# Kernel tuning notes

Measured on AMD Instinct MI355X. Metric: run time of the kernel, lower is better.

## Reference

```python
import jax, jax.numpy as jnp
import numpy as np

D = 1024
H = 16
B = 4
L = 1024
EPS = 1e-5


def _ln(x, g, b):
    m = jnp.mean(x, axis=-1, keepdims=True)
    v = jnp.mean((x - m) ** 2, axis=-1, keepdims=True)
    return (x - m) / jnp.sqrt(v + EPS) * g + b


def _bn_eval(x, g, b, mean, var):
    # x: [B, L, C]; per-channel batchnorm in eval mode
    return (x - mean) / jnp.sqrt(var + EPS) * g + b


def setup_inputs() -> dict:
    key = jax.random.key(0)
    ks = jax.random.split(key, 16)
    s = 0.02
    return {
        "q": jax.random.normal(ks[0], (B, L, D), jnp.float32),
        "wq": jax.random.normal(ks[1], (D, D), jnp.float32) * s,
        "bq": jax.random.normal(ks[2], (D,), jnp.float32) * s,
        "wk": jax.random.normal(ks[3], (D, D), jnp.float32) * s,
        "bk": jax.random.normal(ks[4], (D,), jnp.float32) * s,
        "wv": jax.random.normal(ks[5], (D, D), jnp.float32) * s,
        "bv": jax.random.normal(ks[6], (D,), jnp.float32) * s,
        "wo": jax.random.normal(ks[7], (D, D), jnp.float32) * s,
        "bo": jax.random.normal(ks[8], (D,), jnp.float32) * s,
        "w1": jax.random.normal(ks[9], (4 * D, D), jnp.float32) * s,
        "bn1_g": jax.random.uniform(ks[10], (4 * D,), jnp.float32, 0.5, 1.5),
        "bn1_b": jax.random.normal(ks[11], (4 * D,), jnp.float32) * s,
        "bn1_m": jax.random.normal(ks[12], (4 * D,), jnp.float32) * s,
        "bn1_v": jax.random.uniform(ks[13], (4 * D,), jnp.float32, 0.5, 1.5),
        "w2": jax.random.normal(ks[14], (D, 4 * D), jnp.float32) * s,
        "bn2_g": jax.random.uniform(ks[15], (D,), jnp.float32, 0.5, 1.5),
        "bn2_b": jnp.zeros((D,), jnp.float32),
        "bn2_m": jnp.zeros((D,), jnp.float32),
        "bn2_v": jnp.ones((D,), jnp.float32),
        "ln1_g": jnp.ones((D,), jnp.float32),
        "ln1_b": jnp.zeros((D,), jnp.float32),
        "ln3_g": jnp.ones((D,), jnp.float32),
        "ln3_b": jnp.zeros((D,), jnp.float32),
    }


def reference(q, wq, bq, wk, bk, wv, bv, wo, bo,
              w1, bn1_g, bn1_b, bn1_m, bn1_v,
              w2, bn2_g, bn2_b, bn2_m, bn2_v,
              ln1_g, ln1_b, ln3_g, ln3_b):
    hd = D // H
    scale = hd ** -0.5
    # conv1x1 projections == per-token linear: [B,L,D] @ [D,D]^T + bias
    qp = (q @ wq.T + bq).reshape(B, L, H, hd)
    kp = (q @ wk.T + bk).reshape(B, L, H, hd)
    vp = (q @ wv.T + bv).reshape(B, L, H, hd)
    attn = jnp.einsum('blhd,bmhd->bhlm', qp, kp) * scale  # [B,H,L,L]
    attn = jax.nn.softmax(attn, axis=-1)
    out = jnp.einsum('bhlm,bmhd->blhd', attn, vp).reshape(B, L, D)
    out = out @ wo.T + bo
    # post-norm residual block (norm_first=False, use_residual=True)
    x = _ln(q + out, ln1_g, ln1_b)
    # conv-MLP: 1x1 conv -> BN(eval) -> GELU(exact) -> 1x1 conv -> BN(eval)
    h = x @ w1.T                                   # [B,L,4D]
    h = jax.nn.gelu(_bn_eval(h, bn1_g, bn1_b, bn1_m, bn1_v), approximate=False)
    h = _bn_eval(h @ w2.T, bn2_g, bn2_b, bn2_m, bn2_v)  # [B,L,D]
    x = _ln(x + h, ln3_g, ln3_b)
    return x
```

## Files before the change

kernel.cpp:

```cpp
#include <hip/hip_runtime.h>
#include <math.h>

#define EPS 1e-5f

typedef unsigned short ushort_t;
typedef __attribute__((ext_vector_type(8))) __bf16 bf16x8;
typedef __attribute__((ext_vector_type(4))) __bf16 bf16x4;
typedef __attribute__((ext_vector_type(4))) float f32x4;

#define MFMA16(a, b, c) __builtin_amdgcn_mfma_f32_16x16x32_bf16(a, b, c, 0, 0, 0)

#define QSCALE2 0.18033688011112042f

__device__ __forceinline__ unsigned short f2bf(float f) {
  unsigned u = __float_as_uint(f);
  u += 0x7fffu + ((u >> 16) & 1u);
  return (unsigned short)(u >> 16);
}

__device__ __forceinline__ void gload16(const void* g, void* l) {
  __builtin_amdgcn_global_load_lds(
      (__attribute__((address_space(1))) void*)(g),
      (__attribute__((address_space(3))) void*)(l), 16, 0, 0);
}

__global__ __launch_bounds__(256) void cast_all_k(
    const float* __restrict__ wq, const float* __restrict__ wk,
    const float* __restrict__ wv, const float* __restrict__ wo,
    const float* __restrict__ w1, const float* __restrict__ w2,
    const float* __restrict__ q, ushort_t* __restrict__ wqkv,
    ushort_t* __restrict__ wob, ushort_t* __restrict__ w1b,
    ushort_t* __restrict__ w2b, ushort_t* __restrict__ qbf) {
  const int b = blockIdx.x;
  const float* src;
  ushort_t* dst;
  int idx;
  if (b < 2048) {
    const int s = b >> 9;
    src = (s == 0) ? wq : (s == 1) ? wk : (s == 2) ? wv : wo;
    dst = (s == 3) ? wob : wqkv + s * 1048576;
    idx = (b & 511) * 2048 + threadIdx.x * 8;
  } else if (b < 4096) {
    src = w1; dst = w1b; idx = (b - 2048) * 2048 + threadIdx.x * 8;
  } else if (b < 6144) {
    src = w2; dst = w2b; idx = (b - 4096) * 2048 + threadIdx.x * 8;
  } else {
    src = q; dst = qbf; idx = (b - 6144) * 2048 + threadIdx.x * 8;
  }
  float4 a = *(const float4*)(src + idx);
  float4 c = *(const float4*)(src + idx + 4);
  uint4 u;
  u.x = (unsigned)f2bf(a.x) | ((unsigned)f2bf(a.y) << 16);
  u.y = (unsigned)f2bf(a.z) | ((unsigned)f2bf(a.w) << 16);
  u.z = (unsigned)f2bf(c.x) | ((unsigned)f2bf(c.y) << 16);
  u.w = (unsigned)f2bf(c.z) | ((unsigned)f2bf(c.w) << 16);
  *(uint4*)(dst + idx) = u;
}

__global__ __launch_bounds__(256) void bnparam_k(
    const float* __restrict__ g1, const float* __restrict__ b1,
    const float* __restrict__ m1, const float* __restrict__ v1,
    const float* __restrict__ g2, const float* __restrict__ b2,
    const float* __restrict__ m2, const float* __restrict__ v2,
    float* __restrict__ sc1, float* __restrict__ sh1,
    float* __restrict__ sc2, float* __restrict__ sh2) {
  int i = blockIdx.x * 256 + threadIdx.x;
  if (i < 4096) {
    float s = g1[i] * rsqrtf(v1[i] + EPS);
    sc1[i] = s;
    sh1[i] = b1[i] - m1[i] * s;
  } else if (i < 5120) {
    int j = i - 4096;
    float s = g2[j] * rsqrtf(v2[j] + EPS);
    sc2[j] = s;
    sh2[j] = b2[j] - m2[j] * s;
  }
}

template <int KDIM, int EPI, int TM, int TN, int WM, int WN, int NTHR, int GX, int GY>
__global__ __launch_bounds__(NTHR, 2) void gemm_bt(const ushort_t* __restrict__ A,
                                                   const ushort_t* __restrict__ W,
                                                   const float* __restrict__ p0,
                                                   const float* __restrict__ p1,
                                                   const float* __restrict__ p2,
                                                   float* __restrict__ outF,
                                                   ushort_t* __restrict__ outB) {
  constexpr int BM = 16 * TM * WM, BN = 16 * TN * WN;
  constexpr int LDS_STAGE = 2 * (BM + BN) * 128;
  constexpr int LDS_TR = (EPI == 0) ? 128 * 136 * 2 : 0;
  __shared__ alignas(16) char pool[(LDS_STAGE > LDS_TR) ? LDS_STAGE : LDS_TR];
  constexpr int LA = BM * 8 / NTHR;
  constexpr int LB = BN * 8 / NTHR;

  constexpr int NWG = GX * GY;
  const int id = blockIdx.x;
  const int pos = (id & 7) * (NWG / 8) + (id >> 3);
  const int grp = pos / (8 * GX);
  const int rem = pos % (8 * GX);
  const int by = grp * 8 + (rem & 7);
  const int bx = rem >> 3;
  const int bm = by * BM, bn = bx * BN;

  const int tid = threadIdx.x;
  const int lane = tid & 63;
  const int wid = tid >> 6;
  const int wr = wid / WN, wc = wid % WN;
  const int fr = lane & 15;
  const int kg = lane >> 4;

  const char* Ag0 = (const char*)(A + (size_t)bm * KDIM);
  const char* Bg0 = (const char*)(W + (size_t)bn * KDIM);

#define STAGE(bufi, t_)                                                        \
  do {                                                                         \
    const char* Ag = Ag0 + (size_t)(t_)*128;                                   \
    const char* Bg = Bg0 + (size_t)(t_)*128;                                   \
    char* Ab = pool + (bufi) * (BM * 128);                                     \
    char* Bb = pool + 2 * BM * 128 + (bufi) * (BN * 128);                      \
    _Pragma("unroll") for (int li = 0; li < LA; ++li) {                        \
      const int f = li * NTHR + tid;                                           \
      const int row = f >> 3;                                                  \
      const int gl = (f & 7) ^ (row & 7);                                      \
      gload16(Ag + (size_t)row * (KDIM * 2) + gl * 16,                         \
              Ab + (li * NTHR + wid * 64) * 16);                               \
    }                                                                          \
    _Pragma("unroll") for (int li = 0; li < LB; ++li) {                        \
      const int f = li * NTHR + tid;                                           \
      const int row = f >> 3;                                                  \
      const int gl = (f & 7) ^ (row & 7);                                      \
      gload16(Bg + (size_t)row * (KDIM * 2) + gl * 16,                         \
              Bb + (li * NTHR + wid * 64) * 16);                               \
    }                                                                          \
  } while (0)

  f32x4 acc[TM][TN];
#pragma unroll
  for (int i = 0; i < TM; ++i)
#pragma unroll
    for (int j = 0; j < TN; ++j)
#pragma unroll
      for (int r = 0; r < 4; ++r) acc[i][j][r] = 0.f;

  STAGE(0, 0);
  asm volatile("s_waitcnt vmcnt(0)" ::: "memory");
  __builtin_amdgcn_s_barrier();

  constexpr int NT = KDIM / 64;
  for (int t = 0; t < NT; ++t) {
    const int b = t & 1;
    if (t + 1 < NT) STAGE(b ^ 1, t + 1);
    const char* Ac = pool + b * (BM * 128);
    const char* Bc = pool + 2 * BM * 128 + b * (BN * 128);
#pragma unroll
    for (int s = 0; s < 2; ++s) {
      bf16x8 bfv[TN];
#pragma unroll
      for (int nf = 0; nf < TN; ++nf) {
        const int row = wc * (16 * TN) + nf * 16 + fr;
        bfv[nf] = *(const bf16x8*)(Bc + row * 128 + (((s * 4 + kg) ^ (row & 7)) * 16));
      }
#pragma unroll
      for (int mf = 0; mf < TM; ++mf) {
        const int row = wr * (16 * TM) + mf * 16 + fr;
        bf16x8 af = *(const bf16x8*)(Ac + row * 128 + (((s * 4 + kg) ^ (row & 7)) * 16));
#pragma unroll
        for (int nf = 0; nf < TN; ++nf) acc[mf][nf] = MFMA16(af, bfv[nf], acc[mf][nf]);
      }
    }
    asm volatile("s_waitcnt vmcnt(0)" ::: "memory");
    __builtin_amdgcn_s_barrier();
  }
#undef STAGE

  if constexpr (EPI == 0) {
    if (bn < 2048) {
#pragma unroll
      for (int mf = 0; mf < TM; ++mf) {
#pragma unroll
        for (int nf = 0; nf < TN; ++nf) {
#pragma unroll
          for (int r = 0; r < 4; ++r) {
            const int m = bm + wr * (16 * TM) + mf * 16 + kg * 4 + r;
            const int n = bn + wc * (16 * TN) + nf * 16 + fr;
            const int sel = n >> 10;
            const int nl = n & 1023;
            float v = acc[mf][nf][r] + ((sel == 0) ? p0[nl] : p1[nl]);
            if (sel == 0) v *= QSCALE2;
            const int b_ = m >> 10, tok = m & 1023;
            const int h_ = nl >> 6, d_ = nl & 63;
            outB[(size_t)sel * 4194304 + (((size_t)(b_ * 16 + h_) * 1024 + tok) * 64 + d_)] =
                f2bf(v);
          }
        }
      }
    } else {
      __syncthreads();
      ushort_t* T = (ushort_t*)pool;
#pragma unroll
      for (int mf = 0; mf < TM; ++mf) {
#pragma unroll
        for (int nf = 0; nf < TN; ++nf) {
          const int ml = wr * (16 * TM) + mf * 16 + kg * 4;
          const int nl = wc * (16 * TN) + nf * 16 + fr;
          const float bias = p2[(bn & 1023) + nl];
          bf16x4 pw;
#pragma unroll
          for (int r = 0; r < 4; ++r) pw[r] = (__bf16)(acc[mf][nf][r] + bias);
          *(bf16x4*)(T + nl * 136 + ml) = pw;
        }
      }
      __syncthreads();
      const int b_ = bm >> 10;
      const int tokb = bm & 1023;
#pragma unroll
      for (int it = 0; it < 8; ++it) {
        const int g = it * 256 + tid;
        const int nl = g >> 4;
        const int m0 = (g & 15) * 8;
        bf16x8 v = *(const bf16x8*)(T + nl * 136 + m0);
        const int nloc = (bn - 2048) + nl;
        const int h_ = nloc >> 6, d_ = nloc & 63;
        *(bf16x8*)(outB + 8388608 + (((size_t)(b_ * 16 + h_) * 64 + d_) << 10) + tokb + m0) = v;
      }
    }
  } else {
#pragma unroll
    for (int mf = 0; mf < TM; ++mf) {
#pragma unroll
      for (int nf = 0; nf < TN; ++nf) {
#pragma unroll
        for (int r = 0; r < 4; ++r) {
          const int m = bm + wr * (16 * TM) + mf * 16 + kg * 4 + r;
          const int n = bn + wc * (16 * TN) + nf * 16 + fr;
          float v = acc[mf][nf][r];
          if constexpr (EPI == 1) {
            v += p0[n] + p1[(size_t)m * 1024 + n];
            outF[(size_t)m * 1024 + n] = v;
          } else if constexpr (EPI == 2) {
            float tt = v * p0[n] + p1[n];
            float u = tt * (0.7978845608f + 0.0356774081f * tt * tt);
            float e = exp2f(u * 2.8853900818f);
            float ge = tt * (1.f - 1.f / (e + 1.f));
            outB[(size_t)m * 4096 + n] = f2bf(ge);
          } else {
            outF[(size_t)m * 1024 + n] = v * p0[n] + p1[n];
          }
        }
      }
    }
  }
}

__global__ __launch_bounds__(512) void attn_k(const ushort_t* __restrict__ qp,
                                              const ushort_t* __restrict__ kp,
                                              const ushort_t* __restrict__ vt,
                                              ushort_t* __restrict__ aout) {
  __shared__ ushort_t Kt[2][4096];
  __shared__ ushort_t Vt[2][4096];
  __shared__ ushort_t P[8][16][72];
  const int tid = threadIdx.x;
  const int lane = tid & 63;
  const int wid = tid >> 6;
  const int fr = lane & 15;
  const int kg = lane >> 4;
  const int id = blockIdx.x;
  const int slot = id >> 3;
  const int bh = ((id & 7) << 3) | (slot >> 3);
  const int qc = slot & 7;
  const int b_ = bh >> 4, h_ = bh & 15;

  const size_t base = (size_t)bh << 10;
  const int qrow = qc * 128 + wid * 16 + fr;
  bf16x8 qf0 = *(const bf16x8*)(qp + ((base + qrow) << 6) + kg * 8);
  bf16x8 qf1 = *(const bf16x8*)(qp + ((base + qrow) << 6) + 32 + kg * 8);

  const int srow = tid >> 3;
  const int sg16 = ((tid & 7) ^ (srow & 7)) * 16;
  const char* kTileB = (const char*)kp + ((size_t)bh << 17);
  const char* vTileB = (const char*)vt + ((size_t)bh << 17);
  const size_t koff = (size_t)srow * 128 + sg16;
  const size_t voff = (size_t)srow * 2048 + sg16;

#define STAGE(bufi, kt_)                                                      \
  do {                                                                        \
    gload16(kTileB + (size_t)(kt_)*8192 + koff, (char*)Kt[bufi] + wid * 1024); \
    gload16(vTileB + (size_t)(kt_)*128 + voff, (char*)Vt[bufi] + wid * 1024);  \
  } while (0)

  f32x4 oacc[4];
#pragma unroll
  for (int d = 0; d < 4; ++d)
#pragma unroll
    for (int r = 0; r < 4; ++r) oacc[d][r] = 0.f;
  float mrun = -3.0e38f, lrun = 0.f;

  STAGE(0, 0);
  __syncthreads();

  for (int kt = 0; kt < 16; ++kt) {
    const int c = kt & 1;
    if (kt < 15) STAGE(c ^ 1, kt + 1);
    const char* Kc = (const char*)Kt[c];
    const char* Vc = (const char*)Vt[c];

    f32x4 sacc[4];
#pragma unroll
    for (int nf = 0; nf < 4; ++nf)
#pragma unroll
      for (int r = 0; r < 4; ++r) sacc[nf][r] = 0.f;
    __builtin_amdgcn_s_setprio(1);
#pragma unroll
    for (int nf = 0; nf < 4; ++nf) {
      const int r_ = nf * 16 + fr;
      const char* kr = Kc + r_ * 128;
      bf16x8 kf0 = *(const bf16x8*)(kr + ((kg ^ (r_ & 7)) * 16));
      bf16x8 kf1 = *(const bf16x8*)(kr + (((kg + 4) ^ (r_ & 7)) * 16));
      sacc[nf] = MFMA16(kf0, qf0, sacc[nf]);
      sacc[nf] = MFMA16(kf1, qf1, sacc[nf]);
    }
    __builtin_amdgcn_s_setprio(0);
    float mx = sacc[0][0];
#pragma unroll
    for (int nf = 0; nf < 4; ++nf)
#pragma unroll
      for (int r = 0; r < 4; ++r) mx = fmaxf(mx, sacc[nf][r]);
    mx = fmaxf(mx, __shfl_xor(mx, 16));
    mx = fmaxf(mx, __shfl_xor(mx, 32));
    const float mn = fmaxf(mrun, mx);
    const float c_ = exp2f(mrun - mn);
    float rs = 0.f;
#pragma unroll
    for (int nf = 0; nf < 4; ++nf) {
      bf16x4 pw;
#pragma unroll
      for (int r = 0; r < 4; ++r) {
        float ev = exp2f(sacc[nf][r] - mn);
        rs += ev;
        pw[r] = (__bf16)ev;
      }
      *(bf16x4*)(&P[wid][fr][nf * 16 + kg * 4]) = pw;
    }
    rs += __shfl_xor(rs, 16);
    rs += __shfl_xor(rs, 32);
    lrun = lrun * c_ + rs;
    mrun = mn;
    float cb[4];
#pragma unroll
    for (int r = 0; r < 4; ++r) cb[r] = __shfl(c_, kg * 4 + r);
#pragma unroll
    for (int d = 0; d < 4; ++d)
#pragma unroll
      for (int r = 0; r < 4; ++r) oacc[d][r] *= cb[r];
    bf16x8 pa0 = *(const bf16x8*)(&P[wid][fr][kg * 8]);
    bf16x8 pa1 = *(const bf16x8*)(&P[wid][fr][32 + kg * 8]);
    __builtin_amdgcn_s_setprio(1);
#pragma unroll
    for (int df = 0; df < 4; ++df) {
      const int r_ = df * 16 + fr;
      const char* vr_ = Vc + r_ * 128;
      bf16x8 vf0 = *(const bf16x8*)(vr_ + ((kg ^ (r_ & 7)) * 16));
      bf16x8 vf1 = *(const bf16x8*)(vr_ + (((kg + 4) ^ (r_ & 7)) * 16));
      oacc[df] = MFMA16(pa0, vf0, oacc[df]);
      oacc[df] = MFMA16(pa1, vf1, oacc[df]);
    }
    __builtin_amdgcn_s_setprio(0);
    __syncthreads();
  }
#undef STAGE

  float linv[4];
#pragma unroll
  for (int r = 0; r < 4; ++r) linv[r] = 1.f / __shfl(lrun, kg * 4 + r);
#pragma unroll
  for (int df = 0; df < 4; ++df) {
#pragma unroll
    for (int r = 0; r < 4; ++r) {
      const int tok = qc * 128 + wid * 16 + kg * 4 + r;
      const int d_ = df * 16 + fr;
      aout[((size_t)(b_ * 1024 + tok) * 16 + h_) * 64 + d_] = f2bf(oacc[df][r] * linv[r]);
    }
  }
}

template <int MODE>
__global__ __launch_bounds__(256) void ln_k(const float* __restrict__ in1,
                                            const float* __restrict__ in2,
                                            const float* __restrict__ g,
                                            const float* __restrict__ bt,
                                            float* __restrict__ outF,
                                            ushort_t* __restrict__ outB) {
  const int row = blockIdx.x;
  const int tid = threadIdx.x;
  const size_t off = (size_t)row * 1024 + tid * 4;
  float4 v = *(const float4*)(in1 + off);
  if (MODE == 1) {
    float4 u = *(const float4*)(in2 + off);
    v.x += u.x; v.y += u.y; v.z += u.z; v.w += u.w;
  }
  float s = v.x + v.y + v.z + v.w;
  float q = v.x * v.x + v.y * v.y + v.z * v.z + v.w * v.w;
#pragma unroll
  for (int o = 32; o > 0; o >>= 1) {
    s += __shfl_down(s, o);
    q += __shfl_down(q, o);
  }
  __shared__ float rs[4], rq[4], stat[2];
  const int wid = tid >> 6, lane = tid & 63;
  if (lane == 0) { rs[wid] = s; rq[wid] = q; }
  __syncthreads();
  if (tid == 0) {
    float S = rs[0] + rs[1] + rs[2] + rs[3];
    float Q = rq[0] + rq[1] + rq[2] + rq[3];
    float mean = S * (1.f / 1024.f);
    float var = Q * (1.f / 1024.f) - mean * mean;
    stat[0] = mean;
    stat[1] = rsqrtf(var + EPS);
  }
  __syncthreads();
  const float mean = stat[0], rstd = stat[1];
  const int c = tid * 4;
  float4 o4;
  o4.x = (v.x - mean) * rstd * g[c] + bt[c];
  o4.y = (v.y - mean) * rstd * g[c + 1] + bt[c + 1];
  o4.z = (v.z - mean) * rstd * g[c + 2] + bt[c + 2];
  o4.w = (v.w - mean) * rstd * g[c + 3] + bt[c + 3];
  *(float4*)(outF + off) = o4;
  if (MODE == 0) {
    ushort4 ub;
    ub.x = f2bf(o4.x); ub.y = f2bf(o4.y); ub.z = f2bf(o4.z); ub.w = f2bf(o4.w);
    *(ushort4*)(outB + off) = ub;
  }
}

extern "C" void kernel_launch(void* const* d_in, const int* in_sizes, int n_in,
                              void* d_out, int out_size, void* d_ws, size_t ws_size,
                              hipStream_t stream) {
  const float* q    = (const float*)d_in[0];
  const float* wq   = (const float*)d_in[1];
  const float* bq   = (const float*)d_in[2];
  const float* wk   = (const float*)d_in[3];
  const float* bk   = (const float*)d_in[4];
  const float* wv   = (const float*)d_in[5];
  const float* bv   = (const float*)d_in[6];
  const float* wo   = (const float*)d_in[7];
  const float* bo   = (const float*)d_in[8];
  const float* w1   = (const float*)d_in[9];
  const float* bn1g = (const float*)d_in[10];
  const float* bn1b = (const float*)d_in[11];
  const float* bn1m = (const float*)d_in[12];
  const float* bn1v = (const float*)d_in[13];
  const float* w2   = (const float*)d_in[14];
  const float* bn2g = (const float*)d_in[15];
  const float* bn2b = (const float*)d_in[16];
  const float* bn2m = (const float*)d_in[17];
  const float* bn2v = (const float*)d_in[18];
  const float* ln1g = (const float*)d_in[19];
  const float* ln1b = (const float*)d_in[20];
  const float* ln3g = (const float*)d_in[21];
  const float* ln3b = (const float*)d_in[22];

  char* ws = (char*)d_ws;
  const size_t MB = 1u << 20;
  ushort_t* wqkv = (ushort_t*)(ws);
  ushort_t* w1b  = (ushort_t*)(ws + 6 * MB);
  ushort_t* w2b  = (ushort_t*)(ws + 14 * MB);
  ushort_t* wob  = (ushort_t*)(ws + 22 * MB);
  float* sc1 = (float*)(ws + 24 * MB);
  float* sh1 = sc1 + 4096;
  float* sc2 = sh1 + 4096;
  float* sh2 = sc2 + 1024;
  ushort_t* qbf  = (ushort_t*)(ws + 25 * MB);
  ushort_t* qp   = (ushort_t*)(ws + 33 * MB);
  ushort_t* aout = (ushort_t*)(ws + 57 * MB);
  ushort_t* xbf  = (ushort_t*)(ws + 65 * MB);
  float*    h2   = (float*)(ws + 73 * MB);
  ushort_t* h1   = (ushort_t*)(ws + 33 * MB);
  float* X = (float*)d_out;

  const int NM = 1024 * 1024;
  cast_all_k<<<8192, 256, 0, stream>>>(wq, wk, wv, wo, w1, w2, q, wqkv, wob, w1b, w2b, qbf);
  bnparam_k<<<20, 256, 0, stream>>>(bn1g, bn1b, bn1m, bn1v, bn2g, bn2b, bn2m, bn2v,
                                    sc1, sh1, sc2, sh2);

  gemm_bt<1024, 0, 4, 4, 2, 2, 256, 24, 32><<<768, 256, 0, stream>>>(
      qbf, wqkv, bq, bk, bv, nullptr, qp);
  attn_k<<<512, 512, 0, stream>>>(qp, qp + 4 * NM, qp + 8 * NM, aout);
  gemm_bt<1024, 1, 4, 2, 2, 2, 256, 16, 32><<<512, 256, 0, stream>>>(
      aout, wob, bo, q, nullptr, X, nullptr);
  ln_k<0><<<4096, 256, 0, stream>>>(X, nullptr, ln1g, ln1b, X, xbf);
  gemm_bt<1024, 2, 8, 4, 2, 4, 512, 16, 16><<<256, 512, 0, stream>>>(
      xbf, w1b, sc1, sh1, nullptr, nullptr, h1);
  gemm_bt<4096, 3, 4, 2, 2, 2, 256, 16, 32><<<512, 256, 0, stream>>>(
      h1, w2b, sc2, sh2, nullptr, h2, nullptr);
  ln_k<1><<<4096, 256, 0, stream>>>(X, h2, ln3g, ln3b, X, nullptr);
}
```

Before: 211.4 us.

## Add dedicated 256x256 ping-pong pipelined GEMM for MLP first layer

Replaces the generic templated GEMM for the 4096x4096x1024 MLP up-projection with a specialized 512-thread kernel using 256x256 tiles, a 128KB double-buffered swizzled LDS pool, and interleaved half-tile global-to-LDS staging with explicit barriers, waitcnt and setprio around MFMA quads. It aims to overlap memory loads with matrix-core work and raise MFMA utilization. The large LDS footprint limits occupancy to one workgroup per CU despite the launch-bounds hint of two, and the fine-grained manual barrier schedule is fragile.

```diff
diff --git a/kernel.cpp b/kernel.cpp
--- a/kernel.cpp
+++ b/kernel.cpp
@@ -249,6 +249,145 @@
       }
     }
   }
+}
+
+template <int KDIM, int GX, int GY>
+__global__ __launch_bounds__(512, 2) void gemm8p_mlp1(
+    const ushort_t* __restrict__ A, const ushort_t* __restrict__ W,
+    const float* __restrict__ sc, const float* __restrict__ sh,
+    ushort_t* __restrict__ outB) {
+  __shared__ alignas(16) char pool[131072];
+
+  constexpr int NWG = GX * GY;
+  const int id = blockIdx.x;
+  const int pos = (id & 7) * (NWG / 8) + (id >> 3);
+  const int grp = pos / (8 * GX);
+  const int rem = pos % (8 * GX);
+  const int by = grp * 8 + (rem & 7);
+  const int bx = rem >> 3;
+  const int bm = by * 256, bn = bx * 256;
+
+  const int tid = threadIdx.x;
+  const int lane = tid & 63;
+  const int wid = tid >> 6;
+  const int wr = wid >> 2;
+  const int wc = wid & 3;
+  const int fr = lane & 15;
+  const int kg = lane >> 4;
+
+  const char* Ag0 = (const char*)(A + (size_t)bm * KDIM);
+  const char* Bg0 = (const char*)(W + (size_t)bn * KDIM);
+
+#define STG8(gbase, dbase, t_)                                                  \
+  _Pragma("unroll") for (int hh = 0; hh < 2; ++hh)                              \
+  _Pragma("unroll") for (int li = 0; li < 2; ++li) {                            \
+    const int f = li * 512 + tid;                                               \
+    const int r = f >> 3;                                                       \
+    const int gl = (f & 7) ^ (r & 7);                                           \
+    gload16(gbase + ((size_t)(hh * 128 + r) * KDIM + (size_t)(t_)*64) * 2 + gl * 16, \
+            dbase + hh * 16384 + (li * 512 + wid * 64) * 16);                   \
+  }
+#define STG_A(j, t_) STG8(Ag0, (pool + (j)*65536), t_)
+#define STG_B(j, t_) STG8(Bg0, (pool + (j)*65536 + 32768), t_)
+
+#define LDA8(j, h, s)                                                           \
+  _Pragma("unroll") for (int mf = 0; mf < 4; ++mf) {                            \
+    const int row = wr * 128 + (h)*64 + mf * 16 + fr;                           \
+    af[mf] = *(const bf16x8*)(pool + (j)*65536 + row * 128 +                    \
+                              ((((s)*4 + kg) ^ (row & 7)) * 16));               \
+  }
+#define LDB8(j, s)                                                              \
+  _Pragma("unroll") for (int nf = 0; nf < 4; ++nf) {                            \
+    const int row = wc * 64 + nf * 16 + fr;                                     \
+    bfv[nf] = *(const bf16x8*)(pool + (j)*65536 + 32768 + row * 128 +           \
+                               ((((s)*4 + kg) ^ (row & 7)) * 16));              \
+  }
+#define QUAD8(h)                                                                \
+  __builtin_amdgcn_s_setprio(1);                                                \
+  _Pragma("unroll") for (int mf = 0; mf < 4; ++mf)                              \
+  _Pragma("unroll") for (int nf = 0; nf < 4; ++nf)                              \
+      acc[(h)*4 + mf][nf] = MFMA16(af[mf], bfv[nf], acc[(h)*4 + mf][nf]);       \
+  __builtin_amdgcn_s_setprio(0);
+#define PBAR __builtin_amdgcn_s_barrier()
+#define LGK asm volatile("s_waitcnt lgkmcnt(0)" ::: "memory")
+
+  f32x4 acc[8][4];
+#pragma unroll
+  for (int i = 0; i < 8; ++i)
+#pragma unroll
+    for (int j = 0; j < 4; ++j)
+#pragma unroll
+      for (int r = 0; r < 4; ++r) acc[i][j][r] = 0.f;
+
+  STG_B(0, 0);
+  STG_A(0, 0);
+  STG_B(1, 1);
+  asm volatile("s_waitcnt vmcnt(4)" ::: "memory");
+  PBAR;
+
+  constexpr int NT = KDIM / 64;
+  constexpr int NIT = NT / 2;
+  for (int it = 0; it < NIT; ++it) {
+    const bool more = (it < NIT - 1);
+    const int t0 = 2 * it, t1 = 2 * it + 1;
+    bf16x8 af[4], bfv[4];
+    LDA8(0, 0, 0); LDB8(0, 0);
+    STG_A(1, t1);
+    PBAR; LGK; QUAD8(0); PBAR;
+    LDA8(0, 1, 0);
+    PBAR; LGK; QUAD8(1); PBAR;
+    LDA8(0, 0, 1); LDB8(0, 1);
+    PBAR; LGK; QUAD8(0); PBAR;
+    LDA8(0, 1, 1);
+    if (more) {
+      STG_B(0, t0 + 2);
+      asm volatile("s_waitcnt vmcnt(4)" ::: "memory");
+    } else {
+      asm volatile("s_waitcnt vmcnt(0)" ::: "memory");
+    }
+    PBAR; LGK; QUAD8(1); PBAR;
+    LDA8(1, 0, 0); LDB8(1, 0);
+    if (more) STG_A(0, t0 + 2);
+    PBAR; LGK; QUAD8(0); PBAR;
+    LDA8(1, 1, 0);
+    PBAR; LGK; QUAD8(1); PBAR;
+    LDA8(1, 0, 1); LDB8(1, 1);
+    PBAR; LGK; QUAD8(0); PBAR;
+    LDA8(1, 1, 1);
+    if (more) {
+      STG_B(1, t1 + 2);
+      asm volatile("s_waitcnt vmcnt(4)" ::: "memory");
+    } else {
+      asm volatile("s_waitcnt vmcnt(0)" ::: "memory");
+    }
+    PBAR; LGK; QUAD8(1); PBAR;
+  }
+
+#pragma unroll
+  for (int mi = 0; mi < 8; ++mi) {
+#pragma unroll
+    for (int nf = 0; nf < 4; ++nf) {
+      const int n = bn + wc * 64 + nf * 16 + fr;
+      const float scn = sc[n], shn = sh[n];
+#pragma unroll
+      for (int r = 0; r < 4; ++r) {
+        const int m = bm + wr * 128 + mi * 16 + kg * 4 + r;
+        float tt = acc[mi][nf][r] * scn + shn;
+        float u = tt * (0.7978845608f + 0.0356774081f * tt * tt);
+        float e = exp2f(u * 2.8853900818f);
+        float ge = tt * (1.f - 1.f / (e + 1.f));
+        outB[(size_t)m * 4096 + n] = f2bf(ge);
+      }
+    }
+  }
+#undef STG8
+#undef STG_A
+#undef STG_B
+#undef LDA8
+#undef LDB8
+#undef QUAD8
+#undef PBAR
+#undef LGK
 }
 
 __global__ __launch_bounds__(512) void attn_k(const ushort_t* __restrict__ qp,
@@ -488,8 +627,7 @@
   gemm_bt<1024, 1, 4, 2, 2, 2, 256, 16, 32><<<512, 256, 0, stream>>>(
       aout, wob, bo, q, nullptr, X, nullptr);
   ln_k<0><<<4096, 256, 0, stream>>>(X, nullptr, ln1g, ln1b, X, xbf);
-  gemm_bt<1024, 2, 8, 4, 2, 4, 512, 16, 16><<<256, 512, 0, stream>>>(
-      xbf, w1b, sc1, sh1, nullptr, nullptr, h1);
+  gemm8p_mlp1<1024, 16, 16><<<256, 512, 0, stream>>>(xbf, w1b, sc1, sh1, h1);
   gemm_bt<4096, 3, 4, 2, 2, 2, 256, 16, 32><<<512, 256, 0, stream>>>(
       h1, w2b, sc2, sh2, nullptr, h2, nullptr);
   ln_k<1><<<4096, 256, 0, stream>>>(X, h2, ln3g, ln3b, X, nullptr);
```

Measured after the change: 213.3 us. About the same (+0.9%).
